# Performance work log

Hardware: AMD Instinct MI355X
Metric: run time of the kernel (lower is better)

The kernel has to match this reference:

```python
import jax, jax.numpy as jnp
import numpy as np
import math

ACCBLOCK = 32
SPLITS = 2


def _mam(x, w, accblock):
    """MAM fully-connected: block-accumulate products along K, then max+min over blocks.
    x: [M, K], w: [K, N]  ->  [M, N] = max_blk(partial) + min_blk(partial)
    Implemented as a scan over blocks with running max/min to avoid a [M, nblk, N] tensor.
    """
    M, K = x.shape
    N = w.shape[1]
    nblk = K // accblock
    assert nblk * accblock == K
    xb = x.reshape(M, nblk, accblock).transpose(1, 0, 2)  # [nblk, M, B]
    wb = w.reshape(nblk, accblock, N)                      # [nblk, B, N]
    big = jnp.asarray(jnp.finfo(x.dtype).max, x.dtype)

    def step(carry, blk):
        mx, mn = carry
        xi, wi = blk                      # [M, B], [B, N]
        s = xi @ wi                       # block partial sum [M, N]
        return (jnp.maximum(mx, s), jnp.minimum(mn, s)), None

    init = (jnp.full((M, N), -big, x.dtype), jnp.full((M, N), big, x.dtype))
    (mx, mn), _ = jax.lax.scan(step, init, (xb, wb))
    return mx + mn


def reference(x, weight, bias):
    # eval mode, vcon_steps=0 -> alpha=1, beta=0; no weight dropout, no output dropout
    in_features = weight.shape[1]
    w = weight.T  # [K, N]
    sub = math.ceil(in_features / SPLITS)
    last = in_features - sub * (SPLITS - 1)
    out = _mam(x[:, :sub], w[:sub], ACCBLOCK)
    for i in range(1, SPLITS - 1):
        out = out + _mam(x[:, i * sub:(i + 1) * sub], w[i * sub:(i + 1) * sub], ACCBLOCK)
    out = out + _mam(x[:, in_features - last:], w[in_features - last:], ACCBLOCK)
    return out + bias[None, :]


def setup_inputs() -> dict:
    key = jax.random.key(0)
    k1, k2, k3 = jax.random.split(key, 3)
    M, K, N = 2048, 4096, 4096
    x = jax.random.normal(k1, (M, K), dtype=jnp.float32)
    weight = jax.random.normal(k2, (N, K), dtype=jnp.float32) * (1.0 / math.sqrt(K))
    bias = jax.random.normal(k3, (N,), dtype=jnp.float32) * (1.0 / math.sqrt(K))
    return {"x": x, "weight": weight, "bias": bias}
```

## Files before the change

kernel.cpp:

```cpp
#include <hip/hip_runtime.h>
#include <cstdint>
#include <cstddef>

typedef __bf16 bf16;
typedef __bf16 bf16x8 __attribute__((ext_vector_type(8)));
typedef float  f32x4  __attribute__((ext_vector_type(4)));
typedef float  f32x8  __attribute__((ext_vector_type(8)));

#define MDIM 2048
#define NDIM 4096
#define KDIM 4096
#define FLOATMAX 3.402823466e38f

__global__ void cvt2_f32_to_bf16(const float* __restrict__ x, const float* __restrict__ w,
                                 bf16* __restrict__ xb, bf16* __restrict__ wb,
                                 int xn8, int wn8) {
    const int stride = gridDim.x * blockDim.x;
    int i = blockIdx.x * blockDim.x + threadIdx.x;
    for (int k = i; k < xn8; k += stride) {
        f32x4 lo = reinterpret_cast<const f32x4*>(x)[2 * k];
        f32x4 hi = reinterpret_cast<const f32x4*>(x)[2 * k + 1];
        f32x8 v = {lo[0], lo[1], lo[2], lo[3], hi[0], hi[1], hi[2], hi[3]};
        reinterpret_cast<bf16x8*>(xb)[k] = __builtin_convertvector(v, bf16x8);
    }
    for (int k = i; k < wn8; k += stride) {
        f32x4 lo = reinterpret_cast<const f32x4*>(w)[2 * k];
        f32x4 hi = reinterpret_cast<const f32x4*>(w)[2 * k + 1];
        f32x8 v = {lo[0], lo[1], lo[2], lo[3], hi[0], hi[1], hi[2], hi[3]};
        reinterpret_cast<bf16x8*>(wb)[k] = __builtin_convertvector(v, bf16x8);
    }
}

__device__ __forceinline__ void g2lds16(const bf16* g, bf16* l) {
    __builtin_amdgcn_global_load_lds(
        (const __attribute__((address_space(1))) uint32_t*)g,
        (__attribute__((address_space(3))) uint32_t*)l, 16, 0, 0);
}

__global__ __launch_bounds__(256, 3) void mam_kernel(
    const bf16* __restrict__ A,
    const bf16* __restrict__ B,
    const float* __restrict__ bias,
    float* __restrict__ out)
{
    __shared__ __align__(16) bf16 sA[2][2][128 * 32];
    __shared__ __align__(16) bf16 sB[2][2][64 * 32];

    const int t    = threadIdx.x;
    const int lane = t & 63;
    const int w    = t >> 6;
    const int wm   = (w >> 1) * 64;
    const int wn   = (w & 1) * 32;

    const int l   = blockIdx.y * 64 + blockIdx.x;
    const int xcd = l & 7;
    const int idx = l >> 3;
    const int xg  = xcd * 8 + (idx & 7);
    const int yg  = idx >> 3;
    const int m0 = yg * 128;
    const int n0 = xg * 64;

    const bf16* gAi[2];
    int ldsA[2];
#pragma unroll
    for (int i = 0; i < 2; ++i) {
        const int r = i * 64 + (t >> 2);
        const int c = (t & 3) ^ ((r >> 1) & 3);
        gAi[i] = A + (size_t)(m0 + r) * KDIM + c * 8;
        ldsA[i] = (i * 256 + t) * 8;
    }
    const int rB = t >> 2;
    const bf16* gB1 = B + (size_t)(n0 + rB) * KDIM + (((t & 3) ^ ((rB >> 1) & 3))) * 8;
    const int ldsB = t * 8;

    const int frow = lane & 15;
    const int q    = lane >> 4;
    int offA[4], offB[2];
#pragma unroll
    for (int i = 0; i < 4; ++i) {
        const int RA = wm + i * 16 + frow;
        offA[i] = RA * 32 + (q ^ ((RA >> 1) & 3)) * 8;
    }
#pragma unroll
    for (int j = 0; j < 2; ++j) {
        const int RB = wn + j * 16 + frow;
        offB[j] = RB * 32 + (q ^ ((RB >> 1) & 3)) * 8;
    }

    const f32x4 kZero = {0.f, 0.f, 0.f, 0.f};
    const int orow = (lane >> 4) * 4;
    const int ocol = lane & 15;

#pragma unroll 1
    for (int phase = 0; phase < 2; ++phase) {
        const size_t kb = (size_t)phase * 2048;

        f32x4 mx[4][2], mn[4][2];
#pragma unroll
        for (int i = 0; i < 4; ++i)
#pragma unroll
            for (int j = 0; j < 2; ++j) {
                mx[i][j] = (f32x4)(-FLOATMAX);
                mn[i][j] = (f32x4)(FLOATMAX);
            }

        auto prefetch = [&](int s, int pb) {
            const size_t so = kb + (size_t)s * 64;
#pragma unroll
            for (int i = 0; i < 2; ++i) {
                g2lds16(gAi[i] + so,      &sA[pb][0][ldsA[i]]);
                g2lds16(gAi[i] + so + 32, &sA[pb][1][ldsA[i]]);
            }
            g2lds16(gB1 + so,      &sB[pb][0][ldsB]);
            g2lds16(gB1 + so + 32, &sB[pb][1][ldsB]);
        };

        auto compute = [&](int pb) {
            bf16x8 aF0[4], aF1[4], bF0[2], bF1[2];
#pragma unroll
            for (int i = 0; i < 4; ++i) {
                aF0[i] = *(const bf16x8*)&sA[pb][0][offA[i]];
                aF1[i] = *(const bf16x8*)&sA[pb][1][offA[i]];
            }
#pragma unroll
            for (int j = 0; j < 2; ++j) {
                bF0[j] = *(const bf16x8*)&sB[pb][0][offB[j]];
                bF1[j] = *(const bf16x8*)&sB[pb][1][offB[j]];
            }
#pragma unroll
            for (int i = 0; i < 4; ++i) {
#pragma unroll
                for (int j = 0; j < 2; ++j) {
                    f32x4 s0 = __builtin_amdgcn_mfma_f32_16x16x32_bf16(
                        aF0[i], bF0[j], kZero, 0, 0, 0);
                    f32x4 s1 = __builtin_amdgcn_mfma_f32_16x16x32_bf16(
                        aF1[i], bF1[j], kZero, 0, 0, 0);
#pragma unroll
                    for (int r = 0; r < 4; ++r) {
                        mx[i][j][r] = fmaxf(fmaxf(mx[i][j][r], s0[r]), s1[r]);
                        mn[i][j][r] = fminf(fminf(mn[i][j][r], s0[r]), s1[r]);
                    }
                }
            }
        };

        prefetch(0, 0);

#pragma unroll 1
        for (int it = 0; it < 16; ++it) {
            __syncthreads();
            prefetch(2 * it + 1, 1);
            compute(0);
            __syncthreads();
            if (it < 15) prefetch(2 * it + 2, 0);
            compute(1);
        }

        if (phase == 0) {
#pragma unroll
            for (int j = 0; j < 2; ++j) {
                const int col = n0 + wn + j * 16 + ocol;
                const float bv = bias[col];
#pragma unroll
                for (int i = 0; i < 4; ++i) {
                    const int row = m0 + wm + i * 16 + orow;
#pragma unroll
                    for (int r = 0; r < 4; ++r)
                        out[(size_t)(row + r) * NDIM + col] = mx[i][j][r] + mn[i][j][r] + bv;
                }
            }
        } else {
#pragma unroll
            for (int j = 0; j < 2; ++j) {
                const int col = n0 + wn + j * 16 + ocol;
#pragma unroll
                for (int i = 0; i < 4; ++i) {
                    const int row = m0 + wm + i * 16 + orow;
#pragma unroll
                    for (int r = 0; r < 4; ++r) {
                        float* p = &out[(size_t)(row + r) * NDIM + col];
                        *p += mx[i][j][r] + mn[i][j][r];
                    }
                }
            }
        }
    }
}

extern "C" void kernel_launch(void* const* d_in, const int* in_sizes, int n_in,
                              void* d_out, int out_size, void* d_ws, size_t ws_size,
                              hipStream_t stream) {
    const float* x    = (const float*)d_in[0];
    const float* wgt  = (const float*)d_in[1];
    const float* bias = (const float*)d_in[2];
    float* out = (float*)d_out;

    bf16* xbf = (bf16*)d_ws;
    bf16* wbf = xbf + (size_t)MDIM * KDIM;

    const int xn8 = (MDIM * KDIM) / 8;
    const int wn8 = (NDIM * KDIM) / 8;
    cvt2_f32_to_bf16<<<dim3(4096), dim3(256), 0, stream>>>(x, wgt, xbf, wbf, xn8, wn8);

    dim3 grid(64, 16);
    mam_kernel<<<grid, dim3(256), 0, stream>>>(xbf, wbf, bias, out);
}
```

Before: 269.9 us.

## Use triple-buffered LDS pipeline with vmcnt-based barriers and register split accumulation

Moves the main loop from a double-buffered to a triple-buffered LDS pipeline. Each step now waits with s_waitcnt vmcnt(6), so two stages of global-to-LDS loads stay in flight while the current stage is computed, and it uses one barrier per 64-wide k-step instead of two. The two K-splits are folded in registers through an acc array, which removes the read-modify-write of the output between phases and the second output pass. In exchange, occupancy is lowered to 2 blocks per CU, and the extra buffer raises LDS use and register pressure.

```diff
diff --git a/kernel.cpp b/kernel.cpp
--- a/kernel.cpp
+++ b/kernel.cpp
@@ -37,14 +37,21 @@
         (__attribute__((address_space(3))) uint32_t*)l, 16, 0, 0);
 }
 
-__global__ __launch_bounds__(256, 3) void mam_kernel(
+__device__ __forceinline__ void pipe_barrier_keep6() {
+    asm volatile("s_waitcnt vmcnt(6)\n\ts_barrier" ::: "memory");
+}
+__device__ __forceinline__ void pipe_barrier_drain() {
+    asm volatile("s_waitcnt vmcnt(0)\n\ts_barrier" ::: "memory");
+}
+
+__global__ __launch_bounds__(256, 2) void mam_kernel(
     const bf16* __restrict__ A,
     const bf16* __restrict__ B,
     const float* __restrict__ bias,
     float* __restrict__ out)
 {
-    __shared__ __align__(16) bf16 sA[2][2][128 * 32];
-    __shared__ __align__(16) bf16 sB[2][2][64 * 32];
+    __shared__ __align__(16) bf16 sA[3][2][128 * 32];
+    __shared__ __align__(16) bf16 sB[3][2][64 * 32];
 
     const int t    = threadIdx.x;
     const int lane = t & 63;
@@ -70,7 +77,7 @@
         ldsA[i] = (i * 256 + t) * 8;
     }
     const int rB = t >> 2;
-    const bf16* gB1 = B + (size_t)(n0 + rB) * KDIM + (((t & 3) ^ ((rB >> 1) & 3))) * 8;
+    const bf16* gB1 = B + (size_t)(n0 + rB) * KDIM + ((t & 3) ^ ((rB >> 1) & 3)) * 8;
     const int ldsB = t * 8;
 
     const int frow = lane & 15;
@@ -88,101 +95,96 @@
     }
 
     const f32x4 kZero = {0.f, 0.f, 0.f, 0.f};
-    const int orow = (lane >> 4) * 4;
-    const int ocol = lane & 15;
-
-#pragma unroll 1
-    for (int phase = 0; phase < 2; ++phase) {
-        const size_t kb = (size_t)phase * 2048;
-
-        f32x4 mx[4][2], mn[4][2];
+
+    f32x4 acc[4][2], mx[4][2], mn[4][2];
+#pragma unroll
+    for (int i = 0; i < 4; ++i)
+#pragma unroll
+        for (int j = 0; j < 2; ++j) {
+            acc[i][j] = kZero;
+            mx[i][j] = (f32x4)(-FLOATMAX);
+            mn[i][j] = (f32x4)(FLOATMAX);
+        }
+
+    auto prefetch = [&](int s, int pb) {
+        const size_t so = (size_t)s * 64;
+#pragma unroll
+        for (int i = 0; i < 2; ++i) {
+            g2lds16(gAi[i] + so,      &sA[pb][0][ldsA[i]]);
+            g2lds16(gAi[i] + so + 32, &sA[pb][1][ldsA[i]]);
+        }
+        g2lds16(gB1 + so,      &sB[pb][0][ldsB]);
+        g2lds16(gB1 + so + 32, &sB[pb][1][ldsB]);
+    };
+
+    auto compute = [&](int pb) {
+        bf16x8 aF0[4], aF1[4], bF0[2], bF1[2];
+#pragma unroll
+        for (int i = 0; i < 4; ++i) {
+            aF0[i] = *(const bf16x8*)&sA[pb][0][offA[i]];
+            aF1[i] = *(const bf16x8*)&sA[pb][1][offA[i]];
+        }
+#pragma unroll
+        for (int j = 0; j < 2; ++j) {
+            bF0[j] = *(const bf16x8*)&sB[pb][0][offB[j]];
+            bF1[j] = *(const bf16x8*)&sB[pb][1][offB[j]];
+        }
+#pragma unroll
+        for (int i = 0; i < 4; ++i) {
+#pragma unroll
+            for (int j = 0; j < 2; ++j) {
+                f32x4 s0 = __builtin_amdgcn_mfma_f32_16x16x32_bf16(
+                    aF0[i], bF0[j], kZero, 0, 0, 0);
+                f32x4 s1 = __builtin_amdgcn_mfma_f32_16x16x32_bf16(
+                    aF1[i], bF1[j], kZero, 0, 0, 0);
+#pragma unroll
+                for (int r = 0; r < 4; ++r) {
+                    mx[i][j][r] = fmaxf(fmaxf(mx[i][j][r], s0[r]), s1[r]);
+                    mn[i][j][r] = fminf(fminf(mn[i][j][r], s0[r]), s1[r]);
+                }
+            }
+        }
+    };
+
+    auto fold = [&]() {
 #pragma unroll
         for (int i = 0; i < 4; ++i)
 #pragma unroll
             for (int j = 0; j < 2; ++j) {
+                acc[i][j] += mx[i][j] + mn[i][j];
                 mx[i][j] = (f32x4)(-FLOATMAX);
                 mn[i][j] = (f32x4)(FLOATMAX);
             }
-
-        auto prefetch = [&](int s, int pb) {
-            const size_t so = kb + (size_t)s * 64;
-#pragma unroll
-            for (int i = 0; i < 2; ++i) {
-                g2lds16(gAi[i] + so,      &sA[pb][0][ldsA[i]]);
-                g2lds16(gAi[i] + so + 32, &sA[pb][1][ldsA[i]]);
-            }
-            g2lds16(gB1 + so,      &sB[pb][0][ldsB]);
-            g2lds16(gB1 + so + 32, &sB[pb][1][ldsB]);
-        };
-
-        auto compute = [&](int pb) {
-            bf16x8 aF0[4], aF1[4], bF0[2], bF1[2];
-#pragma unroll
-            for (int i = 0; i < 4; ++i) {
-                aF0[i] = *(const bf16x8*)&sA[pb][0][offA[i]];
-                aF1[i] = *(const bf16x8*)&sA[pb][1][offA[i]];
-            }
-#pragma unroll
-            for (int j = 0; j < 2; ++j) {
-                bF0[j] = *(const bf16x8*)&sB[pb][0][offB[j]];
-                bF1[j] = *(const bf16x8*)&sB[pb][1][offB[j]];
-            }
-#pragma unroll
-            for (int i = 0; i < 4; ++i) {
-#pragma unroll
-                for (int j = 0; j < 2; ++j) {
-                    f32x4 s0 = __builtin_amdgcn_mfma_f32_16x16x32_bf16(
-                        aF0[i], bF0[j], kZero, 0, 0, 0);
-                    f32x4 s1 = __builtin_amdgcn_mfma_f32_16x16x32_bf16(
-                        aF1[i], bF1[j], kZero, 0, 0, 0);
-#pragma unroll
-                    for (int r = 0; r < 4; ++r) {
-                        mx[i][j][r] = fmaxf(fmaxf(mx[i][j][r], s0[r]), s1[r]);
-                        mn[i][j][r] = fminf(fminf(mn[i][j][r], s0[r]), s1[r]);
-                    }
-                }
-            }
-        };
-
-        prefetch(0, 0);
-
+    };
+
+    prefetch(0, 0);
+    prefetch(1, 1);
+
+    int pb = 0;
+    int pf = 2;
 #pragma unroll 1
-        for (int it = 0; it < 16; ++it) {
-            __syncthreads();
-            prefetch(2 * it + 1, 1);
-            compute(0);
-            __syncthreads();
-            if (it < 15) prefetch(2 * it + 2, 0);
-            compute(1);
-        }
-
-        if (phase == 0) {
-#pragma unroll
-            for (int j = 0; j < 2; ++j) {
-                const int col = n0 + wn + j * 16 + ocol;
-                const float bv = bias[col];
-#pragma unroll
-                for (int i = 0; i < 4; ++i) {
-                    const int row = m0 + wm + i * 16 + orow;
-#pragma unroll
-                    for (int r = 0; r < 4; ++r)
-                        out[(size_t)(row + r) * NDIM + col] = mx[i][j][r] + mn[i][j][r] + bv;
-                }
-            }
-        } else {
-#pragma unroll
-            for (int j = 0; j < 2; ++j) {
-                const int col = n0 + wn + j * 16 + ocol;
-#pragma unroll
-                for (int i = 0; i < 4; ++i) {
-                    const int row = m0 + wm + i * 16 + orow;
-#pragma unroll
-                    for (int r = 0; r < 4; ++r) {
-                        float* p = &out[(size_t)(row + r) * NDIM + col];
-                        *p += mx[i][j][r] + mn[i][j][r];
-                    }
-                }
-            }
+    for (int s = 0; s < 64; ++s) {
+        if (s < 63) pipe_barrier_keep6();
+        else        pipe_barrier_drain();
+        if (s + 2 < 64) prefetch(s + 2, pf);
+        compute(pb);
+        if (s == 31 || s == 63) fold();
+        pb = (pb == 2) ? 0 : pb + 1;
+        pf = (pf == 2) ? 0 : pf + 1;
+    }
+
+    const int orow = (lane >> 4) * 4;
+    const int ocol = lane & 15;
+#pragma unroll
+    for (int j = 0; j < 2; ++j) {
+        const int col = n0 + wn + j * 16 + ocol;
+        const float bv = bias[col];
+#pragma unroll
+        for (int i = 0; i < 4; ++i) {
+            const int row = m0 + wm + i * 16 + orow;
+#pragma unroll
+            for (int r = 0; r < 4; ++r)
+                out[(size_t)(row + r) * NDIM + col] = acc[i][j][r] + bv;
         }
     }
 }
```

Result: faster. 262.9 us (-2.6%).
